# Performance work log

Measured on AMD Instinct MI355X. Metric: run time of the kernel, lower is better.

Reference implementation:

```python
import jax, jax.numpy as jnp
import numpy as np

H = 16   # nheads
WIN = 64 # window_size (= sqrt(n) so the b,h,n//w,n//w,dk view is valid)


def setup_inputs() -> dict:
    key = jax.random.key(0)
    ks = jax.random.split(key, 7)
    b, n, d = 4, 4096, 1024
    q = jax.random.normal(ks[0], (b, n, d), dtype=jnp.float32)
    k = jax.random.normal(ks[1], (b, n, d), dtype=jnp.float32)
    v = jax.random.normal(ks[2], (b, n, d), dtype=jnp.float32)
    # nn.Linear(d, d, bias=False) weights, stored torch-style as (out, in)
    Wq = jax.random.normal(ks[3], (d, d), dtype=jnp.float32) * 0.02
    Wk = jax.random.normal(ks[4], (d, d), dtype=jnp.float32) * 0.02
    Wv = jax.random.normal(ks[5], (d, d), dtype=jnp.float32) * 0.02
    Wo = jax.random.normal(ks[6], (d, d), dtype=jnp.float32) * 0.02
    return {"q": q, "k": k, "v": v, "Wq": Wq, "Wk": Wk, "Wv": Wv, "Wo": Wo, "window": 1}


def _attention(q, k, v, Wq, Wk, Wv, Wo, window):
    b, qn, d = q.shape
    n = k.shape[1]
    dk = d // H
    # torch Linear: x @ W.T
    qh = (q @ Wq.T).reshape(b, qn, H, dk).transpose(0, 2, 1, 3)  # (b,h,qn,dk)
    kh = (k @ Wk.T).reshape(b, n, H, dk).transpose(0, 2, 1, 3)
    vh = (v @ Wv.T).reshape(b, n, H, dk).transpose(0, 2, 1, 3)
    if window and WIN > 0:
        nw = n // WIN  # requires n == nw*nw, as in the torch .view
        qh = qh.reshape(b, H, nw, nw, dk)
        kh = kh.reshape(b, H, nw, nw, dk)
        vh = vh.reshape(b, H, nw, nw, dk)
    scale = jnp.float32(1.0) / jnp.sqrt(jnp.float32(dk))
    attn = jnp.einsum('...qd,...kd->...qk', qh, kh) * scale  # block-local scores
    attn = jax.nn.softmax(attn, axis=-1)
    o = jnp.einsum('...qk,...kd->...qd', attn, vh)
    # torch: attn.transpose(1, -2).contiguous().view(b, qn, d)
    o = jnp.swapaxes(o, 1, -2).reshape(b, qn, d)
    return o @ Wo.T


def reference(q, k, v, Wq, Wk, Wv, Wo, window):
    return _attention(q, k, v, Wq, Wk, Wv, Wo, window)
```

## Files before the change

kernel.cpp:

```cpp
#include <hip/hip_runtime.h>


typedef unsigned short u16;
typedef unsigned int u32;
typedef __bf16 bf16x8 __attribute__((ext_vector_type(8)));
typedef float f32x4 __attribute__((ext_vector_type(4)));
typedef u16 u16x8 __attribute__((ext_vector_type(8)));

__device__ __forceinline__ u16 f2bf(float f) {
  u32 u = __builtin_bit_cast(u32, f);
  u += 0x7fffu + ((u >> 16) & 1u);
  return (u16)(u >> 16);
}

__device__ __forceinline__ void cvt8_store(const float* __restrict__ src,
                                           u16* __restrict__ dst, size_t i) {
  const float4 a = *(const float4*)(src + i);
  const float4 b = *(const float4*)(src + i + 4);
  u16x8 r;
  r[0] = f2bf(a.x); r[1] = f2bf(a.y); r[2] = f2bf(a.z); r[3] = f2bf(a.w);
  r[4] = f2bf(b.x); r[5] = f2bf(b.y); r[6] = f2bf(b.z); r[7] = f2bf(b.w);
  *(u16x8*)(dst + i) = r;
}

__global__ __launch_bounds__(256) void cvt3_kernel(
    const float* __restrict__ q, const float* __restrict__ k,
    const float* __restrict__ v, u16* __restrict__ dst) {
  const float* src = (blockIdx.z == 0) ? q : (blockIdx.z == 1) ? k : v;
  cvt8_store(src, dst + (size_t)blockIdx.z * 16777216,
             ((size_t)blockIdx.x * 256 + threadIdx.x) * 8);
}

__global__ __launch_bounds__(256) void cvtw_kernel(
    const float* __restrict__ Wq, const float* __restrict__ Wk,
    const float* __restrict__ Wv, const float* __restrict__ Wo,
    u16* __restrict__ dst) {
  const float* src = (blockIdx.z == 0) ? Wq : (blockIdx.z == 1) ? Wk
                   : (blockIdx.z == 2) ? Wv : Wo;
  cvt8_store(src, dst + (size_t)blockIdx.z * 1048576,
             ((size_t)blockIdx.x * 256 + threadIdx.x) * 8);
}

__device__ __forceinline__ void cp16(const u16* g, u16* l) {
  __builtin_amdgcn_global_load_lds((const __attribute__((address_space(1))) void*)g,
                                   (__attribute__((address_space(3))) void*)l, 16, 0, 0);
}

__device__ __forceinline__ void gemm_core(const u16* __restrict__ A,
                                          const u16* __restrict__ B,
                                          void* __restrict__ Cv, int cf) {
  constexpr int N = 1024, K = 1024;
  __shared__ u16 lA[128 * 32];
  __shared__ u16 lB[128 * 32];
  const int tid = threadIdx.x;
  const int lane = tid & 63, w = tid >> 6;
  const int quad = lane >> 4, lr = lane & 15;
  const int lid = blockIdx.x;
  const int xcd = lid & 7, slot = lid >> 3;
  const int m0 = (xcd * 16 + (slot >> 3)) * 128;
  const int n0 = (slot & 7) * 128;
  const int wr = (w >> 1) * 64, wc = (w & 1) * 64;

  const int ch1 = tid, ch2 = tid + 256;
  const u16* Ag1 = A + (size_t)(m0 + (ch1 >> 2)) * K + (ch1 & 3) * 8;
  const u16* Ag2 = A + (size_t)(m0 + (ch2 >> 2)) * K + (ch2 & 3) * 8;
  const u16* Bg1 = B + (size_t)(n0 + (ch1 >> 2)) * K + (ch1 & 3) * 8;
  const u16* Bg2 = B + (size_t)(n0 + (ch2 >> 2)) * K + (ch2 & 3) * 8;

  f32x4 acc[4][4] = {};
  for (int k0 = 0; k0 < K; k0 += 32) {
    cp16(Ag1 + k0, &lA[ch1 * 8]);
    cp16(Ag2 + k0, &lA[ch2 * 8]);
    cp16(Bg1 + k0, &lB[ch1 * 8]);
    cp16(Bg2 + k0, &lB[ch2 * 8]);
    __syncthreads();
    bf16x8 afr[4], bfr[4];
#pragma unroll
    for (int mi = 0; mi < 4; ++mi)
      afr[mi] = *(const bf16x8*)&lA[(wr + mi * 16 + lr) * 32 + quad * 8];
#pragma unroll
    for (int ni = 0; ni < 4; ++ni)
      bfr[ni] = *(const bf16x8*)&lB[(wc + ni * 16 + lr) * 32 + quad * 8];
#pragma unroll
    for (int mi = 0; mi < 4; ++mi)
#pragma unroll
      for (int ni = 0; ni < 4; ++ni)
        acc[mi][ni] = __builtin_amdgcn_mfma_f32_16x16x32_bf16(afr[mi], bfr[ni], acc[mi][ni], 0, 0, 0);
    __syncthreads();
  }
#pragma unroll
  for (int mi = 0; mi < 4; ++mi)
#pragma unroll
    for (int r = 0; r < 4; ++r) {
      const int row = m0 + wr + mi * 16 + quad * 4 + r;
      if (!cf) {
        u16* dst = (u16*)Cv + (size_t)row * N + n0 + wc + lr;
#pragma unroll
        for (int ni = 0; ni < 4; ++ni) dst[ni * 16] = f2bf(acc[mi][ni][r]);
      } else {
        float* dst = (float*)Cv + (size_t)row * N + n0 + wc + lr;
#pragma unroll
        for (int ni = 0; ni < 4; ++ni) dst[ni * 16] = acc[mi][ni][r];
      }
    }
}

__global__ __launch_bounds__(256, 2) void gemm_qkv_kernel(
    const u16* __restrict__ ws, const u16* __restrict__ Wb,
    u16* __restrict__ Xq, u16* __restrict__ Xk, u16* __restrict__ Xv) {
  const int z = blockIdx.z;
  const u16* A = ws + (size_t)z * 16777216;
  const u16* B = Wb + (size_t)z * 1048576;
  u16* C = (z == 0) ? Xq : (z == 1) ? Xk : Xv;
  gemm_core(A, B, C, 0);
}

__global__ __launch_bounds__(256, 2) void gemm_o_kernel(
    const u16* __restrict__ A, const u16* __restrict__ B,
    float* __restrict__ C) {
  gemm_core(A, B, C, 1);
}

__global__ __launch_bounds__(64) void attn_win_kernel(
    const u16* __restrict__ Xq, const u16* __restrict__ Xk, const u16* __restrict__ Xv,
    u16* __restrict__ Xo) {
  __shared__ u16 P[64 * 72];
  const int bx = blockIdx.x;
  const int wi = bx & 63, h = (bx >> 6) & 15, b = bx >> 10;
  const int lane = threadIdx.x & 63, quad = lane >> 4, lr = lane & 15;
  const size_t tb = (size_t)b * 4096 + wi * 64;
  const u16* qb = Xq + tb * 1024 + h * 64;
  const u16* kb = Xk + tb * 1024 + h * 64;
  const u16* vb = Xv + tb * 1024 + h * 64;

  bf16x8 aq[4][2], bk[4][2];
#pragma unroll
  for (int mi = 0; mi < 4; ++mi)
#pragma unroll
    for (int ks = 0; ks < 2; ++ks) {
      aq[mi][ks] = *(const bf16x8*)(qb + (size_t)(mi * 16 + lr) * 1024 + ks * 32 + quad * 8);
      bk[mi][ks] = *(const bf16x8*)(kb + (size_t)(mi * 16 + lr) * 1024 + ks * 32 + quad * 8);
    }
  f32x4 s[4][4];
#pragma unroll
  for (int mi = 0; mi < 4; ++mi)
#pragma unroll
    for (int ni = 0; ni < 4; ++ni) {
      f32x4 z = {0.f, 0.f, 0.f, 0.f};
      z = __builtin_amdgcn_mfma_f32_16x16x32_bf16(aq[mi][0], bk[ni][0], z, 0, 0, 0);
      s[mi][ni] = __builtin_amdgcn_mfma_f32_16x16x32_bf16(aq[mi][1], bk[ni][1], z, 0, 0, 0);
    }

  u16x8 bvr[2][4];
#pragma unroll
  for (int ks = 0; ks < 2; ++ks)
#pragma unroll
    for (int ci = 0; ci < 4; ++ci) {
      const u16* vc = vb + (size_t)(ks * 32 + quad * 8) * 1024 + ci * 16 + lr;
#pragma unroll
      for (int j = 0; j < 8; ++j) bvr[ks][ci][j] = vc[(size_t)j * 1024];
    }

  const float sc = 0.125f;
#pragma unroll
  for (int mi = 0; mi < 4; ++mi)
#pragma unroll
    for (int r = 0; r < 4; ++r) {
      float mx = fmaxf(fmaxf(s[mi][0][r], s[mi][1][r]), fmaxf(s[mi][2][r], s[mi][3][r]));
#pragma unroll
      for (int m = 1; m < 16; m <<= 1) mx = fmaxf(mx, __shfl_xor(mx, m));
      float sum = 0.f;
#pragma unroll
      for (int ni = 0; ni < 4; ++ni) {
        float p = __expf((s[mi][ni][r] - mx) * sc);
        s[mi][ni][r] = p;
        sum += p;
      }
#pragma unroll
      for (int m = 1; m < 16; m <<= 1) sum += __shfl_xor(sum, m);
      const float inv = 1.f / sum;
#pragma unroll
      for (int ni = 0; ni < 4; ++ni) s[mi][ni][r] *= inv;
    }

#pragma unroll
  for (int mi = 0; mi < 4; ++mi)
#pragma unroll
    for (int ni = 0; ni < 4; ++ni)
#pragma unroll
      for (int r = 0; r < 4; ++r)
        P[(mi * 16 + quad * 4 + r) * 72 + ni * 16 + lr] = f2bf(s[mi][ni][r]);
  __syncthreads();

  f32x4 o[4][4] = {};
#pragma unroll
  for (int ks = 0; ks < 2; ++ks) {
    bf16x8 ap[4];
#pragma unroll
    for (int mi = 0; mi < 4; ++mi)
      ap[mi] = *(const bf16x8*)&P[(mi * 16 + lr) * 72 + ks * 32 + quad * 8];
#pragma unroll
    for (int mi = 0; mi < 4; ++mi)
#pragma unroll
      for (int ci = 0; ci < 4; ++ci)
        o[mi][ci] = __builtin_amdgcn_mfma_f32_16x16x32_bf16(
            ap[mi], __builtin_bit_cast(bf16x8, bvr[ks][ci]), o[mi][ci], 0, 0, 0);
  }

#pragma unroll
  for (int mi = 0; mi < 4; ++mi)
#pragma unroll
    for (int r = 0; r < 4; ++r) {
      const int qp = mi * 16 + quad * 4 + r;
      u16* dst = Xo + ((size_t)b * 4096 + (size_t)qp * 64 + wi) * 1024 + h * 64 + lr;
#pragma unroll
      for (int ci = 0; ci < 4; ++ci) dst[ci * 16] = f2bf(o[mi][ci][r]);
    }
}

extern "C" void kernel_launch(void* const* d_in, const int* in_sizes, int n_in,
                              void* d_out, int out_size, void* d_ws, size_t ws_size,
                              hipStream_t stream) {
  (void)in_sizes; (void)n_in; (void)out_size; (void)ws_size;
  const float* q  = (const float*)d_in[0];
  const float* k  = (const float*)d_in[1];
  const float* v  = (const float*)d_in[2];
  const float* Wq = (const float*)d_in[3];
  const float* Wk = (const float*)d_in[4];
  const float* Wv = (const float*)d_in[5];
  const float* Wo = (const float*)d_in[6];

  constexpr size_t ELEMS = (size_t)16384 * 1024;
  u16* qkvb = (u16*)d_ws;
  u16* Xo   = (u16*)d_ws;
  u16* Wb   = (u16*)d_in[0];
  u16* Xq   = (u16*)d_out;
  u16* Xk   = (u16*)d_out + ELEMS;
  u16* Xv   = (u16*)d_in[2];

  cvt3_kernel<<<dim3(8192, 1, 3), 256, 0, stream>>>(q, k, v, qkvb);
  cvtw_kernel<<<dim3(512, 1, 4), 256, 0, stream>>>(Wq, Wk, Wv, Wo, Wb);
  gemm_qkv_kernel<<<dim3(1024, 1, 3), 256, 0, stream>>>(qkvb, Wb, Xq, Xk, Xv);
  attn_win_kernel<<<dim3(4096), 64, 0, stream>>>(Xq, Xk, Xv, Xo);
  gemm_o_kernel<<<dim3(1024), 256, 0, stream>>>(Xo, Wb + 3145728, (float*)d_out);
}
```

Baseline: 425.5 us.

## Stop writing into input buffers; split QKV GEMM into three launches with workspace reuse

The buffer plan changes so that inputs q and v are no longer overwritten as scratch. Intermediates now rotate through three workspace slots and the output buffer, and the batched QKV GEMM becomes three sequential launches. The activation conversion kernel uses a grid-stride loop over all three tensors in one 2048-block launch, and the Wo conversion moves to just before the output GEMM. This looks mainly like a correctness or safety change, since inputs stay intact across calls, and it adds launch overhead plus less concurrency in the QKV GEMM.

```diff
diff --git a/kernel.cpp b/kernel.cpp
--- a/kernel.cpp
+++ b/kernel.cpp
@@ -23,22 +23,31 @@
   *(u16x8*)(dst + i) = r;
 }
 
-__global__ __launch_bounds__(256) void cvt3_kernel(
+__global__ __launch_bounds__(256) void cvt3s_kernel(
     const float* __restrict__ q, const float* __restrict__ k,
-    const float* __restrict__ v, u16* __restrict__ dst) {
-  const float* src = (blockIdx.z == 0) ? q : (blockIdx.z == 1) ? k : v;
-  cvt8_store(src, dst + (size_t)blockIdx.z * 16777216,
-             ((size_t)blockIdx.x * 256 + threadIdx.x) * 8);
-}
-
-__global__ __launch_bounds__(256) void cvtw_kernel(
+    const float* __restrict__ v, u16* __restrict__ ws) {
+  const int g = blockIdx.x * 256 + threadIdx.x;
+#pragma unroll
+  for (int z = 0; z < 3; ++z) {
+    const float* src = (z == 0) ? q : (z == 1) ? k : v;
+    u16* dst = ws + (size_t)z * 16777216;
+#pragma unroll
+    for (int i = 0; i < 4; ++i)
+      cvt8_store(src, dst, ((size_t)g + (size_t)i * 524288) * 8);
+  }
+}
+
+__global__ __launch_bounds__(256) void cvtw3_kernel(
     const float* __restrict__ Wq, const float* __restrict__ Wk,
-    const float* __restrict__ Wv, const float* __restrict__ Wo,
-    u16* __restrict__ dst) {
-  const float* src = (blockIdx.z == 0) ? Wq : (blockIdx.z == 1) ? Wk
-                   : (blockIdx.z == 2) ? Wv : Wo;
+    const float* __restrict__ Wv, u16* __restrict__ dst) {
+  const float* src = (blockIdx.z == 0) ? Wq : (blockIdx.z == 1) ? Wk : Wv;
   cvt8_store(src, dst + (size_t)blockIdx.z * 1048576,
              ((size_t)blockIdx.x * 256 + threadIdx.x) * 8);
+}
+
+__global__ __launch_bounds__(256) void cvtwo_kernel(
+    const float* __restrict__ Wo, u16* __restrict__ dst) {
+  cvt8_store(Wo, dst, ((size_t)blockIdx.x * 256 + threadIdx.x) * 8);
 }
 
 __device__ __forceinline__ void cp16(const u16* g, u16* l) {
@@ -105,17 +114,13 @@
     }
 }
 
-__global__ __launch_bounds__(256, 2) void gemm_qkv_kernel(
-    const u16* __restrict__ ws, const u16* __restrict__ Wb,
-    u16* __restrict__ Xq, u16* __restrict__ Xk, u16* __restrict__ Xv) {
-  const int z = blockIdx.z;
-  const u16* A = ws + (size_t)z * 16777216;
-  const u16* B = Wb + (size_t)z * 1048576;
-  u16* C = (z == 0) ? Xq : (z == 1) ? Xk : Xv;
+__global__ __launch_bounds__(256, 2) void gemm_bf_kernel(
+    const u16* __restrict__ A, const u16* __restrict__ B,
+    u16* __restrict__ C) {
   gemm_core(A, B, C, 0);
 }
 
-__global__ __launch_bounds__(256, 2) void gemm_o_kernel(
+__global__ __launch_bounds__(256, 2) void gemm_of_kernel(
     const u16* __restrict__ A, const u16* __restrict__ B,
     float* __restrict__ C) {
   gemm_core(A, B, C, 1);
@@ -231,16 +236,18 @@
   const float* Wo = (const float*)d_in[6];
 
   constexpr size_t ELEMS = (size_t)16384 * 1024;
-  u16* qkvb = (u16*)d_ws;
-  u16* Xo   = (u16*)d_ws;
-  u16* Wb   = (u16*)d_in[0];
-  u16* Xq   = (u16*)d_out;
-  u16* Xk   = (u16*)d_out + ELEMS;
-  u16* Xv   = (u16*)d_in[2];
-
-  cvt3_kernel<<<dim3(8192, 1, 3), 256, 0, stream>>>(q, k, v, qkvb);
-  cvtw_kernel<<<dim3(512, 1, 4), 256, 0, stream>>>(Wq, Wk, Wv, Wo, Wb);
-  gemm_qkv_kernel<<<dim3(1024, 1, 3), 256, 0, stream>>>(qkvb, Wb, Xq, Xk, Xv);
-  attn_win_kernel<<<dim3(4096), 64, 0, stream>>>(Xq, Xk, Xv, Xo);
-  gemm_o_kernel<<<dim3(1024), 256, 0, stream>>>(Xo, Wb + 3145728, (float*)d_out);
-}
+  u16* ws0 = (u16*)d_ws;
+  u16* ws1 = ws0 + ELEMS;
+  u16* ws2 = ws1 + ELEMS;
+  u16* do0 = (u16*)d_out;
+  u16* do1 = do0 + ELEMS;
+
+  cvt3s_kernel<<<2048, 256, 0, stream>>>(q, k, v, ws0);
+  cvtw3_kernel<<<dim3(512, 1, 3), 256, 0, stream>>>(Wq, Wk, Wv, do1);
+  gemm_bf_kernel<<<1024, 256, 0, stream>>>(ws0, do1,           do0);
+  gemm_bf_kernel<<<1024, 256, 0, stream>>>(ws1, do1 + 1048576, ws0);
+  gemm_bf_kernel<<<1024, 256, 0, stream>>>(ws2, do1 + 2097152, ws1);
+  attn_win_kernel<<<dim3(4096), 64, 0, stream>>>(do0, ws0, ws1, ws2);
+  cvtwo_kernel<<<512, 256, 0, stream>>>(Wo, ws0);
+  gemm_of_kernel<<<1024, 256, 0, stream>>>(ws2, ws0, (float*)d_out);
+}
```

Measured after the change: 457.7 us. 7.6% more time.
